# Kernel tuning notes

Hardware: AMD Instinct MI355X
Metric: run time of the kernel (lower is better)

The kernel has to match this reference:

```python
import jax, jax.numpy as jnp
import numpy as np

P = 5.0  # p-norm order from init_kwargs


def setup_inputs() -> dict:
    key = jax.random.key(0)
    k1, k2 = jax.random.split(key)
    B, N, M, C = 8, 4096, 4096, 3
    x = jax.random.normal(k1, (B, N, C), dtype=jnp.float32)
    y = jax.random.normal(k2, (B, M, C), dtype=jnp.float32)
    return {"x": x, "y": y}


def _pnorm(v, axis):
    # (sum |v|^p)^(1/p), matching torch.norm(p=5)
    return jnp.sum(jnp.abs(v) ** P, axis=axis) ** (1.0 / P)


def reference(x, y):
    # Squared Euclidean distance matrix [B, N, M]
    d = (-2.0 * jnp.einsum("bnc,bmc->bnm", x, y)
         + jnp.sum(x * x, -1)[:, :, None]
         + jnp.sum(y * y, -1)[:, None, :])
    idx1 = jnp.argmin(d, axis=2)  # [B, N]: nearest y for each x
    idx2 = jnp.argmin(d, axis=1)  # [B, M]: nearest x for each y
    nn_y = jnp.take_along_axis(y, idx1[..., None], axis=1)  # [B, N, 3]
    nn_x = jnp.take_along_axis(x, idx2[..., None], axis=1)  # [B, M, 3]
    pc1 = _pnorm(x - nn_y, axis=-1)  # [B, N]
    pc2 = _pnorm(y - nn_x, axis=-1)  # [B, M]
    result2 = _pnorm(pc1, axis=-1) + _pnorm(pc2, axis=-1)  # [B]
    return jnp.mean(result2)
```

## Files before the change

kernel.cpp:

```cpp
#include <hip/hip_runtime.h>
#include <math.h>


#define BQ      256
#define QPT     2
#define QP      (QPT / 2)
#define SPLITS  16
#define CH      256
#define GS      8
#define NG      (CH / GS)
#define BIGOFF  64.0f
#define NQTOT   65536
#define NTILE   128
#define TILEQ   512

typedef float f32x2 __attribute__((ext_vector_type(2)));

static __device__ __forceinline__ f32x2 mk2(float s) { f32x2 v; v.x = s; v.y = s; return v; }
static __device__ __forceinline__ f32x2 fma2(f32x2 a, f32x2 b, f32x2 c) {
    return __builtin_elementwise_fma(a, b, c);
}
static __device__ __forceinline__ f32x2 min2(f32x2 a, f32x2 b) {
    return __builtin_elementwise_min(a, b);
}
__device__ __forceinline__ unsigned int float_ord(float f) {
    unsigned int u = __float_as_uint(f);
    return (u & 0x80000000u) ? ~u : (u | 0x80000000u);
}

#define WS_ACC    0
#define WS_CANARY 128
#define WS_GCNT   192
#define WS_TCNT   256
#define WS_PSUM   1024
#define WS_TAB    4096

__global__ __launch_bounds__(BQ, 8) void chamfer_fused_r11(
    const float* __restrict__ x, const float* __restrict__ y,
    unsigned long long* __restrict__ tab,
    unsigned int* __restrict__ tcnt, unsigned int* __restrict__ gcnt,
    const unsigned int* __restrict__ canary_p,
    float* __restrict__ psum, float* __restrict__ out)
{
    __shared__ float4 sref[CH];
    __shared__ float red[4];
    __shared__ int s_flag;

    const int bid   = blockIdx.x;
    const int split = bid & (SPLITS - 1);
    const int tq    = bid >> 4;
    const int dir   = tq >> 6;
    const int b     = (tq >> 3) & 7;
    const int t8    = tq & 7;

    const unsigned int canary = *canary_p;

    const float* Q; const float* R;
    if (dir == 0) { Q = x + (size_t)b * 4096 * 3; R = y + (size_t)b * 4096 * 3; }
    else          { Q = y + (size_t)b * 4096 * 3; R = x + (size_t)b * 4096 * 3; }

    const int tid = threadIdx.x;

    if (tid < CH / 2) {
        const float* rp = R + (size_t)(split * CH + 2 * tid) * 3;
        const float f0 = rp[0], f1 = rp[1], f2 = rp[2];
        const float f3 = rp[3], f4 = rp[4], f5 = rp[5];
        const float h0 = fmaf(0.5f * f0, f0, fmaf(0.5f * f1, f1, fmaf(0.5f * f2, f2, BIGOFF)));
        const float h1 = fmaf(0.5f * f3, f3, fmaf(0.5f * f4, f4, fmaf(0.5f * f5, f5, BIGOFF)));
        sref[2 * tid]     = make_float4(f0, f3, f1, f4);
        sref[2 * tid + 1] = make_float4(f2, f5, h0, h1);
    }

    f32x2 nqx[QP], nqy[QP], nqz[QP];
    #pragma unroll
    for (int p = 0; p < QP; ++p) {
        const int ql0 = t8 * TILEQ + (2 * p) * 256 + tid;
        const int ql1 = ql0 + 256;
        nqx[p].x = -Q[ql0 * 3 + 0]; nqx[p].y = -Q[ql1 * 3 + 0];
        nqy[p].x = -Q[ql0 * 3 + 1]; nqy[p].y = -Q[ql1 * 3 + 1];
        nqz[p].x = -Q[ql0 * 3 + 2]; nqz[p].y = -Q[ql1 * 3 + 2];
    }
    __syncthreads();

    f32x2 best2[QP]; int bgA[QP], bgB[QP];
    #pragma unroll
    for (int p = 0; p < QP; ++p) { best2[p] = mk2(3.4e38f); bgA[p] = 0; bgB[p] = 0; }

    #pragma unroll 2
    for (int g = 0; g < NG; ++g) {
        f32x2 macc[QP];
        #pragma unroll
        for (int p = 0; p < QP; ++p) macc[p] = mk2(3.4e38f);
        #pragma unroll
        for (int k = 0; k < GS / 2; ++k) {
            const float4 a = sref[(g * 4 + k) * 2];
            const float4 c = sref[(g * 4 + k) * 2 + 1];
            const f32x2 rxl = mk2(a.x), rxh = mk2(a.y);
            const f32x2 ryl = mk2(a.z), ryh = mk2(a.w);
            const f32x2 rzl = mk2(c.x), rzh = mk2(c.y);
            const f32x2 hl  = mk2(c.z), hh2 = mk2(c.w);
            #pragma unroll
            for (int p = 0; p < QP; ++p) {
                const f32x2 tA = fma2(nqx[p], rxl, fma2(nqy[p], ryl, fma2(nqz[p], rzl, hl)));
                const f32x2 tB = fma2(nqx[p], rxh, fma2(nqy[p], ryh, fma2(nqz[p], rzh, hh2)));
                macc[p] = min2(macc[p], min2(tA, tB));
            }
        }
        #pragma unroll
        for (int p = 0; p < QP; ++p) {
            const bool cA = macc[p].x < best2[p].x;
            best2[p].x = cA ? macc[p].x : best2[p].x;
            bgA[p]     = cA ? g : bgA[p];
            const bool cB = macc[p].y < best2[p].y;
            best2[p].y = cB ? macc[p].y : best2[p].y;
            bgB[p]     = cB ? g : bgB[p];
        }
    }

    #pragma unroll
    for (int p = 0; p < QP; ++p) {
        #pragma unroll
        for (int hh = 0; hh < 2; ++hh) {
            const float bscore = hh ? best2[p].y : best2[p].x;
            const int   bg     = hh ? bgB[p]     : bgA[p];
            const float qx = hh ? -nqx[p].y : -nqx[p].x;
            const float qy = hh ? -nqy[p].y : -nqy[p].x;
            const float qz = hh ? -nqz[p].y : -nqz[p].x;
            const int basej = split * CH + bg * GS;
            int bj = basej;
            #pragma unroll
            for (int j = GS - 1; j >= 0; --j) {
                const float* rp = R + (size_t)(basej + j) * 3;
                const float rx = rp[0], ry = rp[1], rz = rp[2];
                const float h = fmaf(0.5f * rx, rx, fmaf(0.5f * ry, ry, fmaf(0.5f * rz, rz, BIGOFF)));
                const float s = fmaf(-qx, rx, fmaf(-qy, ry, fmaf(-qz, rz, h)));
                if (s == bscore) bj = basej + j;
            }
            const size_t qidx = (size_t)tq * TILEQ + (2 * p + hh) * 256 + tid;
            const unsigned long long key =
                ~(((unsigned long long)__float_as_uint(bscore) << 32) | (unsigned int)bj);
            atomicMax(&tab[qidx], key);
        }
    }

    __syncthreads();
    if (tid == 0) {
        const unsigned int old = atomicAdd(&tcnt[tq], 1u);
        s_flag = (old == canary + (SPLITS - 1));
    }
    __syncthreads();
    if (!s_flag) return;

    float sthr = 0.0f;
    #pragma unroll
    for (int k = 0; k < QPT; ++k) {
        const int gq = tq * TILEQ + k * 256 + tid;
        const int q  = t8 * TILEQ + k * 256 + tid;
        const unsigned long long w =
            ~__hip_atomic_load(&tab[gq], __ATOMIC_RELAXED, __HIP_MEMORY_SCOPE_AGENT);
        const int j = (int)(unsigned int)w;
        const float dx = Q[q * 3 + 0] - R[(size_t)j * 3 + 0];
        const float dy = Q[q * 3 + 1] - R[(size_t)j * 3 + 1];
        const float dz = Q[q * 3 + 2] - R[(size_t)j * 3 + 2];
        const float ax = fabsf(dx), ay = fabsf(dy), az = fabsf(dz);
        const float ax2 = ax * ax, ay2 = ay * ay, az2 = az * az;
        sthr += ax2 * ax2 * ax + ay2 * ay2 * ay + az2 * az2 * az;
    }
    #pragma unroll
    for (int off = 32; off > 0; off >>= 1) sthr += __shfl_down(sthr, off, 64);
    const int wid = tid >> 6, lane = tid & 63;
    if (lane == 0) red[wid] = sthr;
    __syncthreads();

    if (tid == 0) {
        __hip_atomic_store(&psum[tq], red[0] + red[1] + red[2] + red[3],
                           __ATOMIC_RELAXED, __HIP_MEMORY_SCOPE_AGENT);
        asm volatile("s_waitcnt vmcnt(0)" ::: "memory");
        const unsigned int old = atomicAdd(gcnt, 1u);
        s_flag = (old == canary + (NTILE - 1));
    }
    __syncthreads();
    if (!s_flag) return;

    if (tid < 64) {
        float v = 0.0f;
        if (tid < 16) {
            const int fb = tid >> 1, fdir = tid & 1;
            float a = 0.0f;
            #pragma unroll
            for (int t = 0; t < 8; ++t)
                a += __hip_atomic_load(&psum[fdir * 64 + fb * 8 + t],
                                       __ATOMIC_RELAXED, __HIP_MEMORY_SCOPE_AGENT);
            v = exp2f(0.2f * log2f(a));
        }
        #pragma unroll
        for (int off = 8; off > 0; off >>= 1) v += __shfl_down(v, off, 64);
        if (tid == 0) out[0] = v * 0.125f;
    }
    if (tid < NTILE)
        __hip_atomic_store(&tcnt[tid], canary, __ATOMIC_RELAXED, __HIP_MEMORY_SCOPE_AGENT);
    if (tid == 0)
        __hip_atomic_store(gcnt, canary, __ATOMIC_RELAXED, __HIP_MEMORY_SCOPE_AGENT);
}

__global__ __launch_bounds__(BQ) void chamfer_nn_split_kernel(
    const float* __restrict__ x, const float* __restrict__ y,
    unsigned long long* __restrict__ packed, int N, int M)
{
    __shared__ float4 sref[1024];
    const int bid = blockIdx.x, split = bid & 3, qb = bid >> 2;
    const int tile = qb & 15, dir = (qb >> 4) & 1, b = qb >> 5;
    const float* Q; const float* R;
    if (dir == 0) { Q = x + (size_t)b * N * 3; R = y + (size_t)b * M * 3; }
    else          { Q = y + (size_t)b * M * 3; R = x + (size_t)b * N * 3; }
    const int tid = threadIdx.x, q = tile * BQ + tid, base = split * 1024;
    for (int j = tid; j < 1024; j += BQ) {
        const float rx = R[(size_t)(base + j) * 3 + 0];
        const float ry = R[(size_t)(base + j) * 3 + 1];
        const float rz = R[(size_t)(base + j) * 3 + 2];
        sref[j] = make_float4(rx, ry, rz, 0.5f * (rx * rx + ry * ry + rz * rz));
    }
    __syncthreads();
    const float qx = Q[q * 3 + 0], qy = Q[q * 3 + 1], qz = Q[q * 3 + 2];
    float best = 3.4e38f; int bestj = base;
    #pragma unroll 8
    for (int j = 0; j < 1024; ++j) {
        const float4 r = sref[j];
        float t = __fmaf_rn(-qx, r.x, r.w);
        t = __fmaf_rn(-qy, r.y, t);
        t = __fmaf_rn(-qz, r.z, t);
        const bool c = t < best;
        best = c ? t : best; bestj = c ? (base + j) : bestj;
    }
    const size_t idx = ((size_t)dir * 8 + b) * (size_t)N + q;
    atomicMin(&packed[idx], ((unsigned long long)float_ord(best) << 32) | (unsigned int)bestj);
}

__global__ __launch_bounds__(BQ) void chamfer_gather_kernel(
    const float* __restrict__ x, const float* __restrict__ y,
    const unsigned long long* __restrict__ packed,
    float* __restrict__ acc, int N, int M)
{
    __shared__ float red[4];
    const int tid = threadIdx.x;
    const size_t gq = (size_t)blockIdx.x * BQ + tid;
    const int dir = (int)(gq / ((size_t)8 * N));
    const size_t rem = gq - (size_t)dir * 8 * N;
    const int b = (int)(rem / N), q = (int)(rem - (size_t)b * N);
    const float* Q; const float* R;
    if (dir == 0) { Q = x + (size_t)b * N * 3; R = y + (size_t)b * M * 3; }
    else          { Q = y + (size_t)b * M * 3; R = x + (size_t)b * N * 3; }
    const int j = (int)(unsigned int)packed[gq];
    const float dx = Q[q * 3 + 0] - R[(size_t)j * 3 + 0];
    const float dy = Q[q * 3 + 1] - R[(size_t)j * 3 + 1];
    const float dz = Q[q * 3 + 2] - R[(size_t)j * 3 + 2];
    const float ax = fabsf(dx), ay = fabsf(dy), az = fabsf(dz);
    const float ax2 = ax * ax, ay2 = ay * ay, az2 = az * az;
    float s = ax2 * ax2 * ax + ay2 * ay2 * ay + az2 * az2 * az;
    #pragma unroll
    for (int off = 32; off > 0; off >>= 1) s += __shfl_down(s, off, 64);
    const int wid = tid >> 6, lane = tid & 63;
    if (lane == 0) red[wid] = s;
    __syncthreads();
    if (tid == 0) atomicAdd(&acc[b * 2 + dir], red[0] + red[1] + red[2] + red[3]);
}

__global__ void chamfer_finalize_kernel(const float* __restrict__ acc,
                                        float* __restrict__ out)
{
    if (threadIdx.x == 0 && blockIdx.x == 0) {
        float total = 0.0f;
        #pragma unroll
        for (int i = 0; i < 16; ++i) total += powf(acc[i], 0.2f);
        *out = total * 0.125f;
    }
}

extern "C" void kernel_launch(void* const* d_in, const int* in_sizes, int n_in,
                              void* d_out, int out_size, void* d_ws, size_t ws_size,
                              hipStream_t stream)
{
    const float* x = (const float*)d_in[0];
    const float* y = (const float*)d_in[1];
    float* out = (float*)d_out;
    const int N = in_sizes[0] / 24;
    const int M = in_sizes[1] / 24;

    const size_t needed = WS_TAB + (size_t)NQTOT * 8;

    if (N == 4096 && M == 4096 && ws_size >= needed) {
        unsigned char* ws = (unsigned char*)d_ws;
        unsigned long long* tab = (unsigned long long*)(ws + WS_TAB);
        unsigned int* tcnt = (unsigned int*)(ws + WS_TCNT);
        unsigned int* gcnt = (unsigned int*)(ws + WS_GCNT);
        const unsigned int* canary = (const unsigned int*)(ws + WS_CANARY);
        float* psum = (float*)(ws + WS_PSUM);
        chamfer_fused_r11<<<NTILE * SPLITS, BQ, 0, stream>>>(
            x, y, tab, tcnt, gcnt, canary, psum, out);
    } else {
        unsigned char* ws = (unsigned char*)d_ws;
        float* acc = (float*)ws;
        unsigned long long* ptab = (unsigned long long*)(ws + 4096);
        const size_t nQ = (size_t)2 * 8 * N;
        hipMemsetAsync(acc, 0, 64, stream);
        hipMemsetAsync(ptab, 0xFF, nQ * 8, stream);
        chamfer_nn_split_kernel<<<(int)(nQ / BQ) * 4, BQ, 0, stream>>>(x, y, ptab, N, M);
        chamfer_gather_kernel<<<(int)(nQ / BQ), BQ, 0, stream>>>(x, y, ptab, acc, N, M);
        chamfer_finalize_kernel<<<1, 64, 0, stream>>>(acc, out);
    }
}
```

Baseline: 88.44 us.

## Precompute packed reference table in prepass and read it from global memory

Adds a small pre-kernel that packs reference points with their half-norm plus offset into a float4 table in the workspace. The main kernel drops its LDS staging and __syncthreads and reads the table directly through uniform global loads, which the compiler may turn into scalar loads. The inner loop is also reorganised so both queries share the same packed reference pair, with the scalar min done per query. This trades LDS traffic and a barrier for an extra launch and global or L2 reads.

```diff
diff --git a/kernel.cpp b/kernel.cpp
--- a/kernel.cpp
+++ b/kernel.cpp
@@ -4,7 +4,6 @@
 
 #define BQ      256
 #define QPT     2
-#define QP      (QPT / 2)
 #define SPLITS  16
 #define CH      256
 #define GS      8
@@ -20,9 +19,6 @@
 static __device__ __forceinline__ f32x2 fma2(f32x2 a, f32x2 b, f32x2 c) {
     return __builtin_elementwise_fma(a, b, c);
 }
-static __device__ __forceinline__ f32x2 min2(f32x2 a, f32x2 b) {
-    return __builtin_elementwise_min(a, b);
-}
 __device__ __forceinline__ unsigned int float_ord(float f) {
     unsigned int u = __float_as_uint(f);
     return (u & 0x80000000u) ? ~u : (u | 0x80000000u);
@@ -34,15 +30,35 @@
 #define WS_TCNT   256
 #define WS_PSUM   1024
 #define WS_TAB    4096
-
-__global__ __launch_bounds__(BQ, 8) void chamfer_fused_r11(
+#define WS_TBL    1048576
+
+__global__ __launch_bounds__(BQ) void chamfer_mktab(
     const float* __restrict__ x, const float* __restrict__ y,
+    float4* __restrict__ tbl)
+{
+    const int t   = blockIdx.x * BQ + threadIdx.x;
+    const int dir = t >> 14;
+    const int b   = (t >> 11) & 7;
+    const int pr  = t & 2047;
+    const float* R = (dir == 0 ? y : x) + (size_t)b * 4096 * 3;
+    const float* rp = R + (size_t)(2 * pr) * 3;
+    const float f0 = rp[0], f1 = rp[1], f2 = rp[2];
+    const float f3 = rp[3], f4 = rp[4], f5 = rp[5];
+    const float h0 = fmaf(0.5f * f0, f0, fmaf(0.5f * f1, f1, fmaf(0.5f * f2, f2, BIGOFF)));
+    const float h1 = fmaf(0.5f * f3, f3, fmaf(0.5f * f4, f4, fmaf(0.5f * f5, f5, BIGOFF)));
+    const size_t o = ((size_t)(dir * 8 + b) * 2048 + pr) * 2;
+    tbl[o]     = make_float4(f0, f3, f1, f4);
+    tbl[o + 1] = make_float4(f2, f5, h0, h1);
+}
+
+__global__ __launch_bounds__(BQ, 8) void chamfer_fused_r12(
+    const float* __restrict__ x, const float* __restrict__ y,
+    const float4* __restrict__ tbl,
     unsigned long long* __restrict__ tab,
     unsigned int* __restrict__ tcnt, unsigned int* __restrict__ gcnt,
     const unsigned int* __restrict__ canary_p,
     float* __restrict__ psum, float* __restrict__ out)
 {
-    __shared__ float4 sref[CH];
     __shared__ float red[4];
     __shared__ int s_flag;
 
@@ -61,86 +77,62 @@
 
     const int tid = threadIdx.x;
 
-    if (tid < CH / 2) {
-        const float* rp = R + (size_t)(split * CH + 2 * tid) * 3;
-        const float f0 = rp[0], f1 = rp[1], f2 = rp[2];
-        const float f3 = rp[3], f4 = rp[4], f5 = rp[5];
-        const float h0 = fmaf(0.5f * f0, f0, fmaf(0.5f * f1, f1, fmaf(0.5f * f2, f2, BIGOFF)));
-        const float h1 = fmaf(0.5f * f3, f3, fmaf(0.5f * f4, f4, fmaf(0.5f * f5, f5, BIGOFF)));
-        sref[2 * tid]     = make_float4(f0, f3, f1, f4);
-        sref[2 * tid + 1] = make_float4(f2, f5, h0, h1);
-    }
-
-    f32x2 nqx[QP], nqy[QP], nqz[QP];
-    #pragma unroll
-    for (int p = 0; p < QP; ++p) {
-        const int ql0 = t8 * TILEQ + (2 * p) * 256 + tid;
-        const int ql1 = ql0 + 256;
-        nqx[p].x = -Q[ql0 * 3 + 0]; nqx[p].y = -Q[ql1 * 3 + 0];
-        nqy[p].x = -Q[ql0 * 3 + 1]; nqy[p].y = -Q[ql1 * 3 + 1];
-        nqz[p].x = -Q[ql0 * 3 + 2]; nqz[p].y = -Q[ql1 * 3 + 2];
-    }
-    __syncthreads();
-
-    f32x2 best2[QP]; int bgA[QP], bgB[QP];
-    #pragma unroll
-    for (int p = 0; p < QP; ++p) { best2[p] = mk2(3.4e38f); bgA[p] = 0; bgB[p] = 0; }
+    const float4* __restrict__ tb =
+        tbl + ((size_t)(dir * 8 + b) * 4096 + (size_t)split * 256);
+
+    const int ql0 = t8 * TILEQ + tid;
+    const int ql1 = ql0 + 256;
+    const float qx0 = Q[ql0 * 3 + 0], qy0 = Q[ql0 * 3 + 1], qz0 = Q[ql0 * 3 + 2];
+    const float qx1 = Q[ql1 * 3 + 0], qy1 = Q[ql1 * 3 + 1], qz1 = Q[ql1 * 3 + 2];
+    const f32x2 nqx0 = mk2(-qx0), nqy0 = mk2(-qy0), nqz0 = mk2(-qz0);
+    const f32x2 nqx1 = mk2(-qx1), nqy1 = mk2(-qy1), nqz1 = mk2(-qz1);
+
+    float best0 = 3.4e38f, best1 = 3.4e38f;
+    int bg0 = 0, bg1 = 0;
 
     #pragma unroll 2
     for (int g = 0; g < NG; ++g) {
-        f32x2 macc[QP];
-        #pragma unroll
-        for (int p = 0; p < QP; ++p) macc[p] = mk2(3.4e38f);
+        float m0 = 3.4e38f, m1 = 3.4e38f;
         #pragma unroll
         for (int k = 0; k < GS / 2; ++k) {
-            const float4 a = sref[(g * 4 + k) * 2];
-            const float4 c = sref[(g * 4 + k) * 2 + 1];
-            const f32x2 rxl = mk2(a.x), rxh = mk2(a.y);
-            const f32x2 ryl = mk2(a.z), ryh = mk2(a.w);
-            const f32x2 rzl = mk2(c.x), rzh = mk2(c.y);
-            const f32x2 hl  = mk2(c.z), hh2 = mk2(c.w);
-            #pragma unroll
-            for (int p = 0; p < QP; ++p) {
-                const f32x2 tA = fma2(nqx[p], rxl, fma2(nqy[p], ryl, fma2(nqz[p], rzl, hl)));
-                const f32x2 tB = fma2(nqx[p], rxh, fma2(nqy[p], ryh, fma2(nqz[p], rzh, hh2)));
-                macc[p] = min2(macc[p], min2(tA, tB));
-            }
+            const float4 a = tb[(g * 4 + k) * 2];
+            const float4 c = tb[(g * 4 + k) * 2 + 1];
+            f32x2 rx; rx.x = a.x; rx.y = a.y;
+            f32x2 ry; ry.x = a.z; ry.y = a.w;
+            f32x2 rz; rz.x = c.x; rz.y = c.y;
+            f32x2 h2; h2.x = c.z; h2.y = c.w;
+            const f32x2 s0 = fma2(nqx0, rx, fma2(nqy0, ry, fma2(nqz0, rz, h2)));
+            const f32x2 s1 = fma2(nqx1, rx, fma2(nqy1, ry, fma2(nqz1, rz, h2)));
+            m0 = fminf(fminf(m0, s0.x), s0.y);
+            m1 = fminf(fminf(m1, s1.x), s1.y);
         }
+        const bool c0 = m0 < best0;
+        best0 = c0 ? m0 : best0;  bg0 = c0 ? g : bg0;
+        const bool c1 = m1 < best1;
+        best1 = c1 ? m1 : best1;  bg1 = c1 ? g : bg1;
+    }
+
+    #pragma unroll
+    for (int hh = 0; hh < 2; ++hh) {
+        const float bscore = hh ? best1 : best0;
+        const int   bg     = hh ? bg1   : bg0;
+        const float qx = hh ? qx1 : qx0;
+        const float qy = hh ? qy1 : qy0;
+        const float qz = hh ? qz1 : qz0;
+        const int basej = split * CH + bg * GS;
+        int bj = basej;
         #pragma unroll
-        for (int p = 0; p < QP; ++p) {
-            const bool cA = macc[p].x < best2[p].x;
-            best2[p].x = cA ? macc[p].x : best2[p].x;
-            bgA[p]     = cA ? g : bgA[p];
-            const bool cB = macc[p].y < best2[p].y;
-            best2[p].y = cB ? macc[p].y : best2[p].y;
-            bgB[p]     = cB ? g : bgB[p];
+        for (int j = GS - 1; j >= 0; --j) {
+            const float* rp = R + (size_t)(basej + j) * 3;
+            const float rx = rp[0], ry = rp[1], rz = rp[2];
+            const float h = fmaf(0.5f * rx, rx, fmaf(0.5f * ry, ry, fmaf(0.5f * rz, rz, BIGOFF)));
+            const float s = fmaf(-qx, rx, fmaf(-qy, ry, fmaf(-qz, rz, h)));
+            if (s == bscore) bj = basej + j;
         }
-    }
-
-    #pragma unroll
-    for (int p = 0; p < QP; ++p) {
-        #pragma unroll
-        for (int hh = 0; hh < 2; ++hh) {
-            const float bscore = hh ? best2[p].y : best2[p].x;
-            const int   bg     = hh ? bgB[p]     : bgA[p];
-            const float qx = hh ? -nqx[p].y : -nqx[p].x;
-            const float qy = hh ? -nqy[p].y : -nqy[p].x;
-            const float qz = hh ? -nqz[p].y : -nqz[p].x;
-            const int basej = split * CH + bg * GS;
-            int bj = basej;
-            #pragma unroll
-            for (int j = GS - 1; j >= 0; --j) {
-                const float* rp = R + (size_t)(basej + j) * 3;
-                const float rx = rp[0], ry = rp[1], rz = rp[2];
-                const float h = fmaf(0.5f * rx, rx, fmaf(0.5f * ry, ry, fmaf(0.5f * rz, rz, BIGOFF)));
-                const float s = fmaf(-qx, rx, fmaf(-qy, ry, fmaf(-qz, rz, h)));
-                if (s == bscore) bj = basej + j;
-            }
-            const size_t qidx = (size_t)tq * TILEQ + (2 * p + hh) * 256 + tid;
-            const unsigned long long key =
-                ~(((unsigned long long)__float_as_uint(bscore) << 32) | (unsigned int)bj);
-            atomicMax(&tab[qidx], key);
-        }
+        const size_t qidx = (size_t)tq * TILEQ + hh * 256 + tid;
+        const unsigned long long key =
+            ~(((unsigned long long)__float_as_uint(bscore) << 32) | (unsigned int)bj);
+        atomicMax(&tab[qidx], key);
     }
 
     __syncthreads();
@@ -286,7 +278,7 @@
     const int N = in_sizes[0] / 24;
     const int M = in_sizes[1] / 24;
 
-    const size_t needed = WS_TAB + (size_t)NQTOT * 8;
+    const size_t needed = WS_TBL + (size_t)32768 * 32;
 
     if (N == 4096 && M == 4096 && ws_size >= needed) {
         unsigned char* ws = (unsigned char*)d_ws;
@@ -295,8 +287,10 @@
         unsigned int* gcnt = (unsigned int*)(ws + WS_GCNT);
         const unsigned int* canary = (const unsigned int*)(ws + WS_CANARY);
         float* psum = (float*)(ws + WS_PSUM);
-        chamfer_fused_r11<<<NTILE * SPLITS, BQ, 0, stream>>>(
-            x, y, tab, tcnt, gcnt, canary, psum, out);
+        float4* tbl = (float4*)(ws + WS_TBL);
+        chamfer_mktab<<<32768 / BQ, BQ, 0, stream>>>(x, y, tbl);
+        chamfer_fused_r12<<<NTILE * SPLITS, BQ, 0, stream>>>(
+            x, y, tbl, tab, tcnt, gcnt, canary, psum, out);
     } else {
         unsigned char* ws = (unsigned char*)d_ws;
         float* acc = (float*)ws;
```

Result: no change. 89.82 us (+1.6%).
